# Kernel tuning notes

Hardware: AMD Instinct MI355X
Metric: run time of the kernel (lower is better)

The kernel has to match this reference:

```python
import jax, jax.numpy as jnp
import numpy as np

N_KERNELS = 5
MUL_FACTOR = 2.0


def setup_inputs() -> dict:
    key = jax.random.key(0)
    k1, k2 = jax.random.split(key)
    X = jax.random.normal(k1, (4096, 512), dtype=jnp.float32)
    Y = jax.random.normal(k2, (4096, 512), dtype=jnp.float32)
    return {"X": X, "Y": Y}


def _mmd(X, Y):
    # multipliers: 2.0 ** (arange(5) - 2) = [0.25, 0.5, 1, 2, 4]
    mults = MUL_FACTOR ** (jnp.arange(N_KERNELS, dtype=jnp.float32) - N_KERNELS // 2)
    Z = jnp.concatenate([X, Y], axis=0)            # [N+M, D]
    n = Z.shape[0]
    # squared euclidean pairwise distances (cdist ** 2)
    sq = jnp.sum(Z * Z, axis=-1)                    # [N+M]
    D2 = sq[:, None] + sq[None, :] - 2.0 * (Z @ Z.T)
    D2 = jnp.maximum(D2, 0.0)                       # [N+M, N+M]
    # bandwidth from detached distances: sum / (n^2 - n)
    bw = jax.lax.stop_gradient(jnp.sum(D2)) / (n * n - n)
    # multi-bandwidth RBF sum over kernels
    K = jnp.sum(jnp.exp(-D2[None, :, :] / (bw * mults)[:, None, None]), axis=0)
    Nx = X.shape[0]
    XX = jnp.mean(K[:Nx, :Nx])
    XY = jnp.mean(K[:Nx, Nx:])
    YY = jnp.mean(K[Nx:, Nx:])
    return XX - 2.0 * XY + YY


def reference(X, Y):
    return _mmd(X, Y)
```

## Files before the change

kernel.cpp:

```cpp
#include <hip/hip_runtime.h>
#include <math.h>

#define N_ROWS 8192
#define NX     4096
#define DIM    512
#define BT     128
#define NT     64
#define NTRI   2080
#define BK     32

typedef __bf16 bf16_t;
typedef bf16_t bf16x8 __attribute__((ext_vector_type(8)));
typedef float  f32x4  __attribute__((ext_vector_type(4)));

#if __has_builtin(__builtin_amdgcn_exp2f)
  #define EXP2F __builtin_amdgcn_exp2f
#else
  #define EXP2F exp2f
#endif


__device__ __forceinline__ const float* zrow(const float* X, const float* Y, int r) {
    return (r < NX) ? (X + (size_t)r * DIM) : (Y + (size_t)(r - NX) * DIM);
}

__device__ __forceinline__ void gload_lds16(const bf16_t* g, bf16_t* l) {
    __builtin_amdgcn_global_load_lds(
        (__attribute__((address_space(1))) void*)(void*)(g),
        (__attribute__((address_space(3))) void*)(void*)(l), 16, 0, 0);
}

__global__ void k_prep(const float* __restrict__ X, const float* __restrict__ Y,
                       bf16_t* __restrict__ Zh, float* __restrict__ sqrow,
                       float* __restrict__ colsum, unsigned* __restrict__ tk1,
                       double* __restrict__ S1acc) {
    int t = threadIdx.x;
    if (blockIdx.x == 0) {
        colsum[t] = 0.f; colsum[t + 256] = 0.f;
        if (t == 0) { *tk1 = 0u; *S1acc = 0.0; }
    }
    int wv = t >> 6, lane = t & 63;
    int row = blockIdx.x * 4 + wv;
    const float4* z4 = (const float4*)zrow(X, Y, row);
    float4 a = z4[lane * 2], b = z4[lane * 2 + 1];
    bf16x8 h;
    h[0] = (bf16_t)a.x; h[1] = (bf16_t)a.y; h[2] = (bf16_t)a.z; h[3] = (bf16_t)a.w;
    h[4] = (bf16_t)b.x; h[5] = (bf16_t)b.y; h[6] = (bf16_t)b.z; h[7] = (bf16_t)b.w;
    *(bf16x8*)(Zh + (size_t)row * DIM + lane * 8) = h;
    float s = a.x*a.x + a.y*a.y + a.z*a.z + a.w*a.w
            + b.x*b.x + b.y*b.y + b.z*b.z + b.w*b.w;
    #pragma unroll
    for (int off = 32; off > 0; off >>= 1) s += __shfl_down(s, off);
    if (lane == 0) sqrow[row] = s;
}

__global__ __launch_bounds__(512) void k_colsum(const bf16_t* __restrict__ Zh,
                                                const float* __restrict__ sqrow,
                                                float* __restrict__ colsum,
                                                float* __restrict__ cvals,
                                                double* __restrict__ S1acc,
                                                unsigned* __restrict__ tk1,
                                                double* __restrict__ acc,
                                                unsigned* __restrict__ tk2) {
    __shared__ float red[8][4][8];
    __shared__ double dred[512];
    __shared__ int is_last;
    int t = threadIdx.x, lane = t & 63, wv = t >> 6;
    int n16 = lane & 15, q16 = lane >> 4;
    int g = blockIdx.x & 15, slab = blockIdx.x >> 4;
    int c0 = g * 32 + q16 * 8;
    float s[8] = {0.f, 0.f, 0.f, 0.f, 0.f, 0.f, 0.f, 0.f};
    #pragma unroll
    for (int it = 0; it < 8; ++it) {
        int r = slab * 1024 + it * 128 + wv * 16 + n16;
        bf16x8 v = *(const bf16x8*)(Zh + (size_t)r * DIM + c0);
        #pragma unroll
        for (int j = 0; j < 8; ++j) s[j] += (float)v[j];
    }
    #pragma unroll
    for (int off = 8; off >= 1; off >>= 1)
        #pragma unroll
        for (int j = 0; j < 8; ++j) s[j] += __shfl_down(s[j], off);
    if (n16 == 0)
        #pragma unroll
        for (int j = 0; j < 8; ++j) red[wv][q16][j] = s[j];
    __syncthreads();
    float oldc = 0.f;
    if (t < 32) {
        int q = t >> 3, j = t & 7;
        float v = 0.f;
        #pragma unroll
        for (int w = 0; w < 8; ++w) v += red[w][q][j];
        oldc = atomicAdd(&colsum[g * 32 + q * 8 + j], v);
    }
    double olds = 0.0;
    if (g == 0) {
        int i = slab * 1024 + t;
        double d = (double)sqrow[i] + (double)sqrow[i + 512];
        #pragma unroll
        for (int off = 32; off > 0; off >>= 1) d += __shfl_down(d, off);
        if (lane == 0) olds = atomicAdd(S1acc, d);
    }
    asm volatile("" :: "v"(oldc), "v"(olds));
    asm volatile("s_waitcnt vmcnt(0)" ::: "memory");
    __syncthreads();
    if (t == 0) is_last = (atomicAdd(tk1, 1u) == 127u);
    __syncthreads();
    if (!is_last) return;
    float cv = atomicAdd(&colsum[t], 0.f);
    dred[t] = (double)cv * (double)cv;
    __syncthreads();
    for (int off = 256; off > 0; off >>= 1) {
        if (t < off) dred[t] += dred[t + off];
        __syncthreads();
    }
    if (t < 8) acc[t * 16] = 0.0;
    if (t == 0) {
        double S1 = atomicAdd(S1acc, 0.0);
        double n = (double)N_ROWS;
        double sumD2 = 2.0 * n * S1 - 2.0 * dred[0];
        double bw = sumD2 / (n * n - n);
        const double LOG2E = 1.4426950408889634;
        double mult = 0.25;
        for (int k = 0; k < 5; ++k) {
            cvals[k] = (float)(-LOG2E / (bw * mult));
            mult *= 2.0;
        }
        *tk2 = 0u;
    }
}

__global__ __launch_bounds__(256, 3) void k_pair(const bf16_t* __restrict__ Zh,
                                                 const float* __restrict__ sqrow,
                                                 const float* __restrict__ cvals,
                                                 double* __restrict__ acc,
                                                 unsigned* __restrict__ tk2,
                                                 float* __restrict__ out) {
    int L0 = blockIdx.x;
    int L = (L0 & 7) * (NTRI / 8) + (L0 >> 3);
    int ti = (int)(NT + 0.5 - sqrt((NT + 0.5) * (NT + 0.5) - 2.0 * (double)L));
    if (ti < 0) ti = 0;
    while (ti > 0 && ti * NT - ti * (ti - 1) / 2 > L) --ti;
    while ((ti + 1) * NT - (ti + 1) * ti / 2 <= L) ++ti;
    int tj = ti + (L - (ti * NT - ti * (ti - 1) / 2));

    __shared__ bf16_t As[3][4096];
    __shared__ bf16_t Bs[3][4096];
    __shared__ float wsum[4];

    int t = threadIdx.x, lane = t & 63, wv = t >> 6;
    int wr = wv >> 1, wc = wv & 1;
    int i0 = ti * BT + wr * 64;
    int j0 = tj * BT + wc * 64;

    const bf16_t* gA[2]; const bf16_t* gB[2];
    {
        int c0 = t, r0 = c0 >> 2, sq0 = c0 & 3, q0 = sq0 ^ ((r0 >> 1) & 3);
        int c1 = 256 + t, r1 = c1 >> 2, sq1 = c1 & 3, q1 = sq1 ^ ((r1 >> 1) & 3);
        gA[0] = Zh + (size_t)(ti * BT + r0) * DIM + q0 * 8;
        gB[0] = Zh + (size_t)(tj * BT + r0) * DIM + q0 * 8;
        gA[1] = Zh + (size_t)(ti * BT + r1) * DIM + q1 * 8;
        gB[1] = Zh + (size_t)(tj * BT + r1) * DIM + q1 * 8;
    }
    int ldsoff0 = (wv * 64) * 8;
    int ldsoff1 = (256 + wv * 64) * 8;

    int n16 = lane & 15, q16 = lane >> 4;
    int aoff[4], boff[4];
    #pragma unroll
    for (int aa = 0; aa < 4; ++aa) {
        int r = 16 * (wr * 4 + aa) + n16;
        aoff[aa] = (r * 4 + (q16 ^ ((r >> 1) & 3))) * 8;
    }
    #pragma unroll
    for (int bb = 0; bb < 4; ++bb) {
        int r = 16 * (wc * 4 + bb) + n16;
        boff[bb] = (r * 4 + (q16 ^ ((r >> 1) & 3))) * 8;
    }

    f32x4 accf[4][4];
    #pragma unroll
    for (int a = 0; a < 4; ++a)
        #pragma unroll
        for (int b = 0; b < 4; ++b)
            accf[a][b] = (f32x4){0.f, 0.f, 0.f, 0.f};

#define STAGE(S) do {                                   \
        int _b = (S) % 3; int _kn = (S) * BK;           \
        gload_lds16(gA[0] + _kn, &As[_b][ldsoff0]);     \
        gload_lds16(gB[0] + _kn, &Bs[_b][ldsoff0]);     \
        gload_lds16(gA[1] + _kn, &As[_b][ldsoff1]);     \
        gload_lds16(gB[1] + _kn, &Bs[_b][ldsoff1]);     \
    } while (0)

#define KSTEP(S, VM, DO_STAGE) do {                                          \
        asm volatile("s_waitcnt vmcnt(" VM ")" ::: "memory");                \
        __builtin_amdgcn_s_barrier();                                        \
        __builtin_amdgcn_sched_barrier(0);                                   \
        if (DO_STAGE) STAGE((S) + 2);                                        \
        const bf16_t* Ab = &As[(S) % 3][0];                                  \
        const bf16_t* Bb = &Bs[(S) % 3][0];                                  \
        bf16x8 a[4], b[4];                                                   \
        _Pragma("unroll")                                                    \
        for (int aa = 0; aa < 4; ++aa) a[aa] = *(const bf16x8*)(Ab + aoff[aa]); \
        _Pragma("unroll")                                                    \
        for (int bb = 0; bb < 4; ++bb) b[bb] = *(const bf16x8*)(Bb + boff[bb]); \
        __builtin_amdgcn_s_setprio(1);                                       \
        _Pragma("unroll")                                                    \
        for (int aa = 0; aa < 4; ++aa)                                       \
            _Pragma("unroll")                                                \
            for (int bb = 0; bb < 4; ++bb)                                   \
                accf[aa][bb] = __builtin_amdgcn_mfma_f32_16x16x32_bf16(      \
                    a[aa], b[bb], accf[aa][bb], 0, 0, 0);                    \
        __builtin_amdgcn_s_setprio(0);                                       \
    } while (0)

    STAGE(0); STAGE(1);
    KSTEP( 0, "4", 1); KSTEP( 1, "4", 1); KSTEP( 2, "4", 1); KSTEP( 3, "4", 1);
    KSTEP( 4, "4", 1); KSTEP( 5, "4", 1); KSTEP( 6, "4", 1); KSTEP( 7, "4", 1);
    KSTEP( 8, "4", 1); KSTEP( 9, "4", 1); KSTEP(10, "4", 1); KSTEP(11, "4", 1);
    KSTEP(12, "4", 1); KSTEP(13, "4", 1);
    KSTEP(14, "4", 0);
    KSTEP(15, "0", 0);
#undef KSTEP
#undef STAGE

    float c4 = cvals[4];
    float sqi[4][4], sqj[4];
    #pragma unroll
    for (int aa = 0; aa < 4; ++aa)
        #pragma unroll
        for (int r = 0; r < 4; ++r)
            sqi[aa][r] = sqrow[i0 + 16 * aa + q16 * 4 + r];
    #pragma unroll
    for (int bb = 0; bb < 4; ++bb)
        sqj[bb] = sqrow[j0 + 16 * bb + n16];

    float s_local = 0.f;
    #pragma unroll
    for (int aa = 0; aa < 4; ++aa) {
        #pragma unroll
        for (int bb = 0; bb < 4; ++bb) {
            #pragma unroll
            for (int r = 0; r < 4; ++r) {
                float d2 = fmaf(-2.f, accf[aa][bb][r], sqi[aa][r] + sqj[bb]);
                d2 = fmaxf(d2, 0.f);
                float e4 = EXP2F(d2 * c4);
                float e3 = e4 * e4;
                float e2 = e3 * e3;
                float e1 = e2 * e2;
                float e0 = e1 * e1;
                s_local += e4 + e3 + e2 + e1 + e0;
            }
        }
    }
    #pragma unroll
    for (int off = 32; off > 0; off >>= 1) s_local += __shfl_down(s_local, off);
    if (lane == 0) wsum[wv] = s_local;
    __syncthreads();
    if (t == 0) {
        float bs = wsum[0] + wsum[1] + wsum[2] + wsum[3];
        double si = (ti < NT / 2) ? 1.0 : -1.0;
        double sj = (tj < NT / 2) ? 1.0 : -1.0;
        double w = si * sj * ((ti == tj) ? 1.0 : 2.0);
        double oldv = atomicAdd(&acc[(L0 & 7) * 16], w * (double)bs);
        asm volatile("" :: "v"(oldv));
        asm volatile("s_waitcnt vmcnt(0)" ::: "memory");
        unsigned old = atomicAdd(tk2, 1u);
        if (old == NTRI - 1) {
            double ssum = 0.0;
            #pragma unroll
            for (int i = 0; i < 8; ++i) ssum += atomicAdd(&acc[i * 16], 0.0);
            out[0] = (float)(ssum / ((double)NX * (double)NX));
        }
    }
}

extern "C" void kernel_launch(void* const* d_in, const int* in_sizes, int n_in,
                              void* d_out, int out_size, void* d_ws, size_t ws_size,
                              hipStream_t stream) {
    const float* X = (const float*)d_in[0];
    const float* Y = (const float*)d_in[1];
    float* out = (float*)d_out;

    float*    sqrow  = (float*)d_ws;
    float*    colsum = sqrow + 8192;
    float*    cvals  = (float*)((char*)d_ws + 34816);
    unsigned* tk1    = (unsigned*)((char*)d_ws + 34840);
    unsigned* tk2    = (unsigned*)((char*)d_ws + 34844);
    double*   S1acc  = (double*)((char*)d_ws + 34848);
    double*   acc    = (double*)((char*)d_ws + 34944);
    bf16_t*   Zh     = (bf16_t*)((char*)d_ws + 36864);

    k_prep  <<<2048, 256, 0, stream>>>(X, Y, Zh, sqrow, colsum, tk1, S1acc);
    k_colsum<<<128, 512, 0, stream>>>(Zh, sqrow, colsum, cvals, S1acc, tk1, acc, tk2);
    k_pair  <<<NTRI, 256, 0, stream>>>(Zh, sqrow, cvals, acc, tk2, out);
}
```

Baseline: 133.2 us.

## Widen pair tiles to 128x256 with paired column tiles per block

Each block now computes a 128x256 tile of the Gram matrix, covering two adjacent 128-column tiles, so the upper-triangle grid drops to 1056 blocks. Partial sums are kept per column half, and a below-diagonal half gets zero weight. The aim is more MFMA work per LDS load of the A tile and fewer blocks, at the cost of a larger accumulator, lower occupancy (launch bounds 2) and some wasted compute on diagonal blocks.

Result: no change. 133.7 us (+0.4%).

```diff
diff --git a/kernel.cpp b/kernel.cpp
--- a/kernel.cpp
+++ b/kernel.cpp
@@ -1,12 +1,10 @@
 #include <hip/hip_runtime.h>
-#include <math.h>
 
 #define N_ROWS 8192
 #define NX     4096
 #define DIM    512
-#define BT     128
 #define NT     64
-#define NTRI   2080
+#define NBLK   1056
 #define BK     32
 
 typedef __bf16 bf16_t;
@@ -130,67 +128,74 @@
     }
 }
 
-__global__ __launch_bounds__(256, 3) void k_pair(const bf16_t* __restrict__ Zh,
+__global__ __launch_bounds__(256, 2) void k_pair(const bf16_t* __restrict__ Zh,
                                                  const float* __restrict__ sqrow,
                                                  const float* __restrict__ cvals,
                                                  double* __restrict__ acc,
                                                  unsigned* __restrict__ tk2,
                                                  float* __restrict__ out) {
     int L0 = blockIdx.x;
-    int L = (L0 & 7) * (NTRI / 8) + (L0 >> 3);
-    int ti = (int)(NT + 0.5 - sqrt((NT + 0.5) * (NT + 0.5) - 2.0 * (double)L));
-    if (ti < 0) ti = 0;
-    while (ti > 0 && ti * NT - ti * (ti - 1) / 2 > L) --ti;
-    while ((ti + 1) * NT - (ti + 1) * ti / 2 <= L) ++ti;
-    int tj = ti + (L - (ti * NT - ti * (ti - 1) / 2));
+    int L = (L0 & 7) * (NBLK / 8) + (L0 >> 3);
+    int ti = 0;
+    while (ti < NT - 1) {
+        int nx = ti + 1, M = nx >> 1;
+        int off = 64 * M - M * (M - 1) + ((nx & 1) ? (32 - M) : 0);
+        if (off <= L) ti = nx; else break;
+    }
+    int Mi = ti >> 1;
+    int offti = 64 * Mi - Mi * (Mi - 1) + ((ti & 1) ? (32 - Mi) : 0);
+    int tc = (ti >> 1) + (L - offti);
 
     __shared__ bf16_t As[3][4096];
-    __shared__ bf16_t Bs[3][4096];
-    __shared__ float wsum[4];
+    __shared__ bf16_t Bs[3][8192];
+    __shared__ float wsum[4][2];
 
     int t = threadIdx.x, lane = t & 63, wv = t >> 6;
     int wr = wv >> 1, wc = wv & 1;
-    int i0 = ti * BT + wr * 64;
-    int j0 = tj * BT + wc * 64;
-
-    const bf16_t* gA[2]; const bf16_t* gB[2];
-    {
-        int c0 = t, r0 = c0 >> 2, sq0 = c0 & 3, q0 = sq0 ^ ((r0 >> 1) & 3);
-        int c1 = 256 + t, r1 = c1 >> 2, sq1 = c1 & 3, q1 = sq1 ^ ((r1 >> 1) & 3);
-        gA[0] = Zh + (size_t)(ti * BT + r0) * DIM + q0 * 8;
-        gB[0] = Zh + (size_t)(tj * BT + r0) * DIM + q0 * 8;
-        gA[1] = Zh + (size_t)(ti * BT + r1) * DIM + q1 * 8;
-        gB[1] = Zh + (size_t)(tj * BT + r1) * DIM + q1 * 8;
-    }
-    int ldsoff0 = (wv * 64) * 8;
-    int ldsoff1 = (256 + wv * 64) * 8;
+    int i0 = ti * 128 + wr * 64;
+    int j0 = tc * 256 + wc * 128;
+
+    const bf16_t* gA[2]; const bf16_t* gB[4];
+    #pragma unroll
+    for (int h = 0; h < 2; ++h) {
+        int c = h * 256 + t, r = c >> 2, q = (c & 3) ^ ((r >> 1) & 3);
+        gA[h] = Zh + (size_t)(ti * 128 + r) * DIM + q * 8;
+    }
+    #pragma unroll
+    for (int h = 0; h < 4; ++h) {
+        int c = h * 256 + t, r = c >> 2, q = (c & 3) ^ ((r >> 1) & 3);
+        gB[h] = Zh + (size_t)(tc * 256 + r) * DIM + q * 8;
+    }
+    int ldsA0 = (wv * 64) * 8, ldsA1 = (256 + wv * 64) * 8;
 
     int n16 = lane & 15, q16 = lane >> 4;
-    int aoff[4], boff[4];
+    int aoff[4], boff[8];
     #pragma unroll
     for (int aa = 0; aa < 4; ++aa) {
-        int r = 16 * (wr * 4 + aa) + n16;
+        int r = wr * 64 + aa * 16 + n16;
         aoff[aa] = (r * 4 + (q16 ^ ((r >> 1) & 3))) * 8;
     }
     #pragma unroll
-    for (int bb = 0; bb < 4; ++bb) {
-        int r = 16 * (wc * 4 + bb) + n16;
+    for (int bb = 0; bb < 8; ++bb) {
+        int r = wc * 128 + bb * 16 + n16;
         boff[bb] = (r * 4 + (q16 ^ ((r >> 1) & 3))) * 8;
     }
 
-    f32x4 accf[4][4];
+    f32x4 accf[4][8];
     #pragma unroll
     for (int a = 0; a < 4; ++a)
         #pragma unroll
-        for (int b = 0; b < 4; ++b)
+        for (int b = 0; b < 8; ++b)
             accf[a][b] = (f32x4){0.f, 0.f, 0.f, 0.f};
 
-#define STAGE(S) do {                                   \
-        int _b = (S) % 3; int _kn = (S) * BK;           \
-        gload_lds16(gA[0] + _kn, &As[_b][ldsoff0]);     \
-        gload_lds16(gB[0] + _kn, &Bs[_b][ldsoff0]);     \
-        gload_lds16(gA[1] + _kn, &As[_b][ldsoff1]);     \
-        gload_lds16(gB[1] + _kn, &Bs[_b][ldsoff1]);     \
+#define STAGE(S) do {                                        \
+        int _b = (S) % 3; int _kn = (S) * BK;                \
+        gload_lds16(gA[0] + _kn, &As[_b][ldsA0]);            \
+        gload_lds16(gA[1] + _kn, &As[_b][ldsA1]);            \
+        gload_lds16(gB[0] + _kn, &Bs[_b][ldsA0]);            \
+        gload_lds16(gB[1] + _kn, &Bs[_b][ldsA1]);            \
+        gload_lds16(gB[2] + _kn, &Bs[_b][ldsA0 + 4096]);     \
+        gload_lds16(gB[3] + _kn, &Bs[_b][ldsA1 + 4096]);     \
     } while (0)
 
 #define KSTEP(S, VM, DO_STAGE) do {                                          \
@@ -200,47 +205,48 @@
         if (DO_STAGE) STAGE((S) + 2);                                        \
         const bf16_t* Ab = &As[(S) % 3][0];                                  \
         const bf16_t* Bb = &Bs[(S) % 3][0];                                  \
-        bf16x8 a[4], b[4];                                                   \
+        bf16x8 a[4], b[8];                                                   \
         _Pragma("unroll")                                                    \
         for (int aa = 0; aa < 4; ++aa) a[aa] = *(const bf16x8*)(Ab + aoff[aa]); \
         _Pragma("unroll")                                                    \
-        for (int bb = 0; bb < 4; ++bb) b[bb] = *(const bf16x8*)(Bb + boff[bb]); \
+        for (int bb = 0; bb < 8; ++bb) b[bb] = *(const bf16x8*)(Bb + boff[bb]); \
         __builtin_amdgcn_s_setprio(1);                                       \
         _Pragma("unroll")                                                    \
         for (int aa = 0; aa < 4; ++aa)                                       \
             _Pragma("unroll")                                                \
-            for (int bb = 0; bb < 4; ++bb)                                   \
+            for (int bb = 0; bb < 8; ++bb)                                   \
                 accf[aa][bb] = __builtin_amdgcn_mfma_f32_16x16x32_bf16(      \
                     a[aa], b[bb], accf[aa][bb], 0, 0, 0);                    \
         __builtin_amdgcn_s_setprio(0);                                       \
     } while (0)
 
     STAGE(0); STAGE(1);
-    KSTEP( 0, "4", 1); KSTEP( 1, "4", 1); KSTEP( 2, "4", 1); KSTEP( 3, "4", 1);
-    KSTEP( 4, "4", 1); KSTEP( 5, "4", 1); KSTEP( 6, "4", 1); KSTEP( 7, "4", 1);
-    KSTEP( 8, "4", 1); KSTEP( 9, "4", 1); KSTEP(10, "4", 1); KSTEP(11, "4", 1);
-    KSTEP(12, "4", 1); KSTEP(13, "4", 1);
-    KSTEP(14, "4", 0);
+    KSTEP( 0, "6", 1); KSTEP( 1, "6", 1); KSTEP( 2, "6", 1); KSTEP( 3, "6", 1);
+    KSTEP( 4, "6", 1); KSTEP( 5, "6", 1); KSTEP( 6, "6", 1); KSTEP( 7, "6", 1);
+    KSTEP( 8, "6", 1); KSTEP( 9, "6", 1); KSTEP(10, "6", 1); KSTEP(11, "6", 1);
+    KSTEP(12, "6", 1); KSTEP(13, "6", 1);
+    KSTEP(14, "6", 0);
     KSTEP(15, "0", 0);
 #undef KSTEP
 #undef STAGE
 
     float c4 = cvals[4];
-    float sqi[4][4], sqj[4];
+    float sqi[4][4], sqj[8];
     #pragma unroll
     for (int aa = 0; aa < 4; ++aa)
         #pragma unroll
         for (int r = 0; r < 4; ++r)
             sqi[aa][r] = sqrow[i0 + 16 * aa + q16 * 4 + r];
     #pragma unroll
-    for (int bb = 0; bb < 4; ++bb)
+    for (int bb = 0; bb < 8; ++bb)
         sqj[bb] = sqrow[j0 + 16 * bb + n16];
 
-    float s_local = 0.f;
+    float s0 = 0.f, s1 = 0.f;
     #pragma unroll
     for (int aa = 0; aa < 4; ++aa) {
         #pragma unroll
-        for (int bb = 0; bb < 4; ++bb) {
+        for (int bb = 0; bb < 8; ++bb) {
+            float part = 0.f;
             #pragma unroll
             for (int r = 0; r < 4; ++r) {
                 float d2 = fmaf(-2.f, accf[aa][bb][r], sqi[aa][r] + sqj[bb]);
@@ -250,24 +256,35 @@
                 float e2 = e3 * e3;
                 float e1 = e2 * e2;
                 float e0 = e1 * e1;
-                s_local += e4 + e3 + e2 + e1 + e0;
+                part += e4 + e3 + e2 + e1 + e0;
             }
+            if ((wc == 0 && bb < 8 && (bb * 16 < 128)) || (wc == 1 && false)) {}
+            if (wc == 0) { if (bb < 8) { if (bb * 16 < 128) s0 += part; } }
+            else s1 += part;
         }
     }
     #pragma unroll
-    for (int off = 32; off > 0; off >>= 1) s_local += __shfl_down(s_local, off);
-    if (lane == 0) wsum[wv] = s_local;
+    for (int off = 32; off > 0; off >>= 1) {
+        s0 += __shfl_down(s0, off);
+        s1 += __shfl_down(s1, off);
+    }
+    if (lane == 0) { wsum[wv][0] = s0; wsum[wv][1] = s1; }
     __syncthreads();
     if (t == 0) {
-        float bs = wsum[0] + wsum[1] + wsum[2] + wsum[3];
-        double si = (ti < NT / 2) ? 1.0 : -1.0;
-        double sj = (tj < NT / 2) ? 1.0 : -1.0;
-        double w = si * sj * ((ti == tj) ? 1.0 : 2.0);
-        double oldv = atomicAdd(&acc[(L0 & 7) * 16], w * (double)bs);
+        float bs0 = wsum[0][0] + wsum[2][0];
+        float bs1 = wsum[1][1] + wsum[3][1];
+        int tj0 = 2 * tc, tj1 = 2 * tc + 1;
+        double si = (ti < 32) ? 1.0 : -1.0;
+        double w0 = (tj0 < ti) ? 0.0
+                  : si * ((tj0 < 32) ? 1.0 : -1.0) * ((tj0 == ti) ? 1.0 : 2.0);
+        double w1 = (tj1 < ti) ? 0.0
+                  : si * ((tj1 < 32) ? 1.0 : -1.0) * ((tj1 == ti) ? 1.0 : 2.0);
+        double v = w0 * (double)bs0 + w1 * (double)bs1;
+        double oldv = atomicAdd(&acc[(L0 & 7) * 16], v);
         asm volatile("" :: "v"(oldv));
         asm volatile("s_waitcnt vmcnt(0)" ::: "memory");
         unsigned old = atomicAdd(tk2, 1u);
-        if (old == NTRI - 1) {
+        if (old == NBLK - 1) {
             double ssum = 0.0;
             #pragma unroll
             for (int i = 0; i < 8; ++i) ssum += atomicAdd(&acc[i * 16], 0.0);
@@ -294,5 +311,5 @@
 
     k_prep  <<<2048, 256, 0, stream>>>(X, Y, Zh, sqrow, colsum, tk1, S1acc);
     k_colsum<<<128, 512, 0, stream>>>(Zh, sqrow, colsum, cvals, S1acc, tk1, acc, tk2);
-    k_pair  <<<NTRI, 256, 0, stream>>>(Zh, sqrow, cvals, acc, tk2, out);
-}
+    k_pair  <<<NBLK, 256, 0, stream>>>(Zh, sqrow, cvals, acc, tk2, out);
+}
```
